# Performance work log

Hardware: AMD Instinct MI355X
Metric: run time of the kernel (lower is better)

Reference implementation:

```python
import jax, jax.numpy as jnp
import numpy as np

MAX_LEN = 512   # static padding cap for the ragged sequences
EPS = 1e-12     # F.normalize default eps


def setup_inputs() -> dict:
    key = jax.random.key(0)
    ks = jax.random.split(key, 6)
    B, T, D, H = 2048, 262144, 64, 128
    x = jax.random.normal(ks[0], (T, D), jnp.float32)
    offsets = jnp.sort(jax.random.randint(ks[1], (B,), 0, T)).astype(jnp.int64)
    offsets = offsets.at[0].set(0)  # first segment starts at 0 as in EmbeddingLookup
    W_ih = jax.random.normal(ks[2], (3 * H, D), jnp.float32) * 0.1   # [r,z,n] stacked
    W_hh = jax.random.normal(ks[3], (3 * H, H), jnp.float32) * 0.1
    W_dense = jax.random.normal(ks[4], (D, H), jnp.float32) * 0.1
    b_dense = jax.random.normal(ks[5], (D,), jnp.float32) * 0.1
    return {"x": x, "offsets": offsets, "W_ih": W_ih, "W_hh": W_hh,
            "W_dense": W_dense, "b_dense": b_dense}


def _forward(x, W_ih, W_hh, W_dense, b_dense, offsets):
    T, D = x.shape
    B = offsets.shape[0]
    H = W_hh.shape[1]
    # segment lengths as in get_field_embedding_list: diffs + trailing segment
    lengths = jnp.concatenate([offsets[1:] - offsets[:-1], T - offsets[-1:]])
    lengths = jnp.clip(lengths, 1, MAX_LEN)
    # ragged -> padded [B, L, D] (pad_sequence equivalent)
    t_idx = jnp.arange(MAX_LEN)
    gidx = jnp.clip(offsets[:, None] + t_idx[None, :], 0, T - 1)      # [B, L]
    mask = (t_idx[None, :] < lengths[:, None]).astype(x.dtype)        # [B, L]
    padded = x[gidx] * mask[:, :, None]                               # [B, L, D]
    # single-layer GRU, bias=False, batch_first; scan over time
    xs = jnp.transpose(padded, (1, 0, 2))                             # [L, B, D]

    def step(h, x_t):
        gi = x_t @ W_ih.T                                             # [B, 3H]
        gh = h @ W_hh.T                                               # [B, 3H]
        ir, iz, inn = jnp.split(gi, 3, axis=-1)
        hr, hz, hn = jnp.split(gh, 3, axis=-1)
        r = jax.nn.sigmoid(ir + hr)
        z = jax.nn.sigmoid(iz + hz)
        n = jnp.tanh(inn + r * hn)
        h_new = (1.0 - z) * n + z * h
        return h_new, h_new

    h0 = jnp.zeros((B, H), x.dtype)
    _, ys = jax.lax.scan(step, h0, xs)                                # [L, B, H]
    gru_out = jnp.transpose(ys, (1, 0, 2))                            # [B, L, H]
    # gather_indexes: hidden state at last valid timestep
    last = gru_out[jnp.arange(B), lengths - 1]                        # [B, H]
    out = last @ W_dense.T + b_dense                                  # [B, D]
    norm = jnp.linalg.norm(out, axis=-1, keepdims=True)
    return out / jnp.maximum(norm, EPS)


def reference(x, offsets, W_ih, W_hh, W_dense, b_dense):
    return _forward(x, W_ih, W_hh, W_dense, b_dense, offsets)
```

## Files before the change

kernel.cpp:

```cpp
#include <hip/hip_runtime.h>
#include <math.h>

constexpr int D = 64;
constexpr int H = 128;
constexpr int MAXLEN = 512;
constexpr int MSEQ = 8;

typedef __attribute__((ext_vector_type(8))) short short8;
typedef __attribute__((ext_vector_type(4))) float f32x4;

__device__ __forceinline__ short f2bf(float f) {
    unsigned u = __float_as_uint(f);
    u += 0x7fffu + ((u >> 16) & 1u);
    return (short)(u >> 16);
}
__device__ __forceinline__ unsigned cvtpk(float a, float b) {
    unsigned r;
    asm volatile("v_cvt_pk_bf16_f32 %0, %1, %2" : "=v"(r) : "v"(a), "v"(b));
    return r;
}
__device__ __forceinline__ short8 pack8(float4 a, float4 b) {
    short8 r;
    r[0]=f2bf(a.x); r[1]=f2bf(a.y); r[2]=f2bf(a.z); r[3]=f2bf(a.w);
    r[4]=f2bf(b.x); r[5]=f2bf(b.y); r[6]=f2bf(b.z); r[7]=f2bf(b.w);
    return r;
}
__device__ __forceinline__ float rcp_(float x) { return __builtin_amdgcn_rcpf(x); }
__device__ __forceinline__ float sig_(float v) { return rcp_(1.0f + __expf(-v)); }
__device__ __forceinline__ float tanh_(float v) {
    float a = fabsf(v);
    float e = __expf(2.0f * a);
    float t = 1.0f - 2.0f * rcp_(e + 1.0f);
    return copysignf(t, v);
}
__device__ __forceinline__ void lgkm_barrier() {
    asm volatile("s_waitcnt lgkmcnt(0)\n\ts_barrier" ::: "memory");
}

#define MFMA(a,b,c) __builtin_amdgcn_mfma_f32_16x16x32_bf16((a),(b),(c),0,0,0)

__global__ __launch_bounds__(256, 1)
void gru_w4(const float* __restrict__ x,
            const int* __restrict__ offsets,
            const float* __restrict__ W_ih,
            const float* __restrict__ W_hh,
            const float* __restrict__ W_dense,
            const float* __restrict__ b_dense,
            float* __restrict__ out,
            int B, int T)
{
    const int bb   = blockIdx.x;
    const int tid  = threadIdx.x;
    const int w    = tid >> 6;
    const int l    = tid & 63;
    const int s    = l & 15;
    const int q    = l >> 4;
    const int sq   = s & 7;
    const int hsel = s >> 3;

    __shared__ __align__(16) short h_bf[2][MSEQ * H];
    __shared__ __align__(16) short x_bf[2][MSEQ * D];
    __shared__ int slen[MSEQ], sstart[MSEQ];
    __shared__ float h_f32[MSEQ][H];

    if (tid < MSEQ) {
        int sg = bb * MSEQ + tid;
        int st = 0, en = 1;
        if (sg < B) { st = offsets[sg]; en = (sg + 1 < B) ? offsets[sg + 1] : T; }
        int ln = en - st;
        ln = max(1, min(ln, MAXLEN));
        sstart[tid] = st; slen[tid] = ln;
    }
    {
        int* hz = (int*)h_bf[0];
        hz[tid] = 0; hz[tid + 256] = 0;
    }
    __syncthreads();

    int nt = 1;
#pragma unroll
    for (int i = 0; i < MSEQ; ++i) nt = max(nt, slen[i]);

    short8 Wh[3][2][4];
    short8 Wi[3][2][2];
#pragma unroll
    for (int g = 0; g < 3; ++g) {
#pragma unroll
        for (int u = 0; u < 2; ++u) {
            const int grow = g * H + w * 32 + u * 16 + s;
            const float* ph = W_hh + (size_t)grow * H + q * 8;
#pragma unroll
            for (int kt = 0; kt < 4; ++kt)
                Wh[g][u][kt] = pack8(*(const float4*)(ph + kt * 32),
                                     *(const float4*)(ph + kt * 32 + 4));
            const float* pi = W_ih + (size_t)grow * D + q * 8;
#pragma unroll
            for (int kt = 0; kt < 2; ++kt)
                Wi[g][u][kt] = pack8(*(const float4*)(pi + kt * 32),
                                     *(const float4*)(pi + kt * 32 + 4));
        }
    }

    int hoff[4], xoff[2], woff[2];
#pragma unroll
    for (int kt = 0; kt < 4; ++kt) hoff[kt] = sq * 256 + (((kt * 4 + q) ^ sq) << 4);
#pragma unroll
    for (int kt = 0; kt < 2; ++kt) xoff[kt] = sq * 128 + (((kt * 4 + q) ^ sq) << 4);
#pragma unroll
    for (int u = 0; u < 2; ++u)
        woff[u] = sq * 256 + ((((4 * w) + (2 * u) + (q >> 1)) ^ sq) << 4)
                + ((q & 1) << 3) + (hsel << 2);

    const int ss  = tid >> 5;
    const int pxx = tid & 31;
    const int st_x = sstart[ss];
    const int ln_x = slen[ss];
    const float* xg = x + (size_t)st_x * D + pxx * 2;
    const int xwoff = ss * 128 + (((pxx >> 2) ^ ss) << 4) + ((pxx & 3) << 2);

    {
        float2 v = *(const float2*)xg;
        *(unsigned*)((char*)x_bf[0] + xwoff) = cvtpk(v.x, v.y);
    }
    float2 xpf = *(const float2*)(xg + (size_t)min(1, ln_x - 1) * D);

    const int ln_s = slen[sq];
    float h00 = 0.f, h01 = 0.f;
    float h10 = 0.f, h11 = 0.f;

    __syncthreads();

    for (int t = 0; t < nt; ++t) {
        const int p = t & 1;
        const char* hb = (const char*)h_bf[p];
        const char* xb = (const char*)x_bf[p];

        short8 bh[4], bx[2];
#pragma unroll
        for (int kt = 0; kt < 4; ++kt) bh[kt] = *(const short8*)(hb + hoff[kt]);
#pragma unroll
        for (int kt = 0; kt < 2; ++kt) bx[kt] = *(const short8*)(xb + xoff[kt]);

        float2 xnew;
        {
            const int tn = (t + 2 < ln_x) ? t + 2 : ln_x - 1;
            xnew = *(const float2*)(xg + (size_t)tn * D);
        }

        f32x4 cr[2] = {{0,0,0,0},{0,0,0,0}};
        f32x4 cz[2] = {{0,0,0,0},{0,0,0,0}};
        f32x4 ci[2] = {{0,0,0,0},{0,0,0,0}};
        f32x4 chh[2]= {{0,0,0,0},{0,0,0,0}};
#pragma unroll
        for (int u = 0; u < 2; ++u) {
#pragma unroll
            for (int kt = 0; kt < 2; ++kt) {
                cr[u] = MFMA(Wi[0][u][kt], bx[kt], cr[u]);
                cz[u] = MFMA(Wi[1][u][kt], bx[kt], cz[u]);
                ci[u] = MFMA(Wi[2][u][kt], bx[kt], ci[u]);
            }
#pragma unroll
            for (int kt = 0; kt < 4; ++kt) {
                cr[u]  = MFMA(Wh[0][u][kt], bh[kt], cr[u]);
                cz[u]  = MFMA(Wh[1][u][kt], bh[kt], cz[u]);
                chh[u] = MFMA(Wh[2][u][kt], bh[kt], chh[u]);
            }
        }

        const bool upd = (t < ln_s);
        {
            float vr0 = hsel ? cr[0][2]  : cr[0][0],  vr1 = hsel ? cr[0][3]  : cr[0][1];
            float vz0 = hsel ? cz[0][2]  : cz[0][0],  vz1 = hsel ? cz[0][3]  : cz[0][1];
            float vi0 = hsel ? ci[0][2]  : ci[0][0],  vi1 = hsel ? ci[0][3]  : ci[0][1];
            float vh0 = hsel ? chh[0][2] : chh[0][0], vh1 = hsel ? chh[0][3] : chh[0][1];
            float r0 = sig_(vr0), r1 = sig_(vr1);
            float z0 = sig_(vz0), z1 = sig_(vz1);
            float n0 = tanh_(vi0 + r0 * vh0);
            float n1 = tanh_(vi1 + r1 * vh1);
            float a0 = (1.0f - z0) * n0 + z0 * h00;
            float a1 = (1.0f - z1) * n1 + z1 * h01;
            h00 = upd ? a0 : h00;
            h01 = upd ? a1 : h01;
        }
        {
            float vr0 = hsel ? cr[1][2]  : cr[1][0],  vr1 = hsel ? cr[1][3]  : cr[1][1];
            float vz0 = hsel ? cz[1][2]  : cz[1][0],  vz1 = hsel ? cz[1][3]  : cz[1][1];
            float vi0 = hsel ? ci[1][2]  : ci[1][0],  vi1 = hsel ? ci[1][3]  : ci[1][1];
            float vh0 = hsel ? chh[1][2] : chh[1][0], vh1 = hsel ? chh[1][3] : chh[1][1];
            float r0 = sig_(vr0), r1 = sig_(vr1);
            float z0 = sig_(vz0), z1 = sig_(vz1);
            float n0 = tanh_(vi0 + r0 * vh0);
            float n1 = tanh_(vi1 + r1 * vh1);
            float a0 = (1.0f - z0) * n0 + z0 * h10;
            float a1 = (1.0f - z1) * n1 + z1 * h11;
            h10 = upd ? a0 : h10;
            h11 = upd ? a1 : h11;
        }

        *(unsigned*)((char*)h_bf[p ^ 1] + woff[0]) = cvtpk(h00, h01);
        *(unsigned*)((char*)h_bf[p ^ 1] + woff[1]) = cvtpk(h10, h11);
        *(unsigned*)((char*)x_bf[p ^ 1] + xwoff)   = cvtpk(xpf.x, xpf.y);
        xpf = xnew;

        lgkm_barrier();
    }

    {
        float2 hv0 = { h00, h01 };
        float2 hv1 = { h10, h11 };
        *(float2*)&h_f32[sq][w * 32 + 0  + q * 4 + 2 * hsel] = hv0;
        *(float2*)&h_f32[sq][w * 32 + 16 + q * 4 + 2 * hsel] = hv1;
    }
    __syncthreads();

    {
        const int s2 = tid >> 5;
        const int cb = tid & 31;
        float acc0 = b_dense[cb];
        float acc1 = b_dense[cb + 32];
        const float* w0 = W_dense + (size_t)cb * H;
        const float* w1 = W_dense + (size_t)(cb + 32) * H;
#pragma unroll
        for (int j = 0; j < H; j += 4) {
            float4 hv = *(const float4*)&h_f32[s2][j];
            float4 a0 = *(const float4*)(w0 + j);
            float4 a1 = *(const float4*)(w1 + j);
            acc0 += hv.x*a0.x + hv.y*a0.y + hv.z*a0.z + hv.w*a0.w;
            acc1 += hv.x*a1.x + hv.y*a1.y + hv.z*a1.z + hv.w*a1.w;
        }
        float s2q = acc0 * acc0 + acc1 * acc1;
#pragma unroll
        for (int off = 16; off >= 1; off >>= 1) s2q += __shfl_xor(s2q, off);
        float invn = 1.0f / fmaxf(sqrtf(s2q), 1e-12f);
        int sg = bb * MSEQ + s2;
        if (sg < B) {
            out[(size_t)sg * D + cb]      = acc0 * invn;
            out[(size_t)sg * D + cb + 32] = acc1 * invn;
        }
    }
}

extern "C" void kernel_launch(void* const* d_in, const int* in_sizes, int n_in,
                              void* d_out, int out_size, void* d_ws, size_t ws_size,
                              hipStream_t stream) {
    const float* x       = (const float*)d_in[0];
    const int*   offsets = (const int*)d_in[1];
    const float* W_ih    = (const float*)d_in[2];
    const float* W_hh    = (const float*)d_in[3];
    const float* W_dense = (const float*)d_in[4];
    const float* b_dense = (const float*)d_in[5];
    float*       out     = (float*)d_out;

    const int B = in_sizes[1];
    const int T = in_sizes[0] / D;
    const int grid = (B + MSEQ - 1) / MSEQ;

    gru_w4<<<grid, 256, 0, stream>>>(x, offsets, W_ih, W_hh, W_dense, b_dense, out, B, T);
}
```

Before: 352.6 us.

## Precompute next-step input projections off the GRU recurrence critical path

Moves the x·W_ih MFMAs for step t+1 to after the gate update of step t, so that each step's dependent path holds only the h·W_hh MFMAs. The x staging buffer is now filled one step further ahead, with two slots primed before the loop and the global prefetch pushed to t+3. The gate accumulators are seeded with the precomputed input projections. The cost is more live accumulator registers and a deeper prefetch with its own edge-case indexing.

```diff
diff --git a/kernel.cpp b/kernel.cpp
--- a/kernel.cpp
+++ b/kernel.cpp
@@ -40,7 +40,7 @@
 #define MFMA(a,b,c) __builtin_amdgcn_mfma_f32_16x16x32_bf16((a),(b),(c),0,0,0)
 
 __global__ __launch_bounds__(256, 1)
-void gru_w4(const float* __restrict__ x,
+void gru_p4(const float* __restrict__ x,
             const int* __restrict__ offsets,
             const float* __restrict__ W_ih,
             const float* __restrict__ W_hh,
@@ -119,10 +119,12 @@
     const int xwoff = ss * 128 + (((pxx >> 2) ^ ss) << 4) + ((pxx & 3) << 2);
 
     {
-        float2 v = *(const float2*)xg;
-        *(unsigned*)((char*)x_bf[0] + xwoff) = cvtpk(v.x, v.y);
-    }
-    float2 xpf = *(const float2*)(xg + (size_t)min(1, ln_x - 1) * D);
+        float2 v0 = *(const float2*)xg;
+        float2 v1 = *(const float2*)(xg + (size_t)min(1, ln_x - 1) * D);
+        *(unsigned*)((char*)x_bf[0] + xwoff) = cvtpk(v0.x, v0.y);
+        *(unsigned*)((char*)x_bf[1] + xwoff) = cvtpk(v1.x, v1.y);
+    }
+    float2 xpf = *(const float2*)(xg + (size_t)min(2, ln_x - 1) * D);
 
     const int ln_s = slen[sq];
     float h00 = 0.f, h01 = 0.f;
@@ -130,49 +132,55 @@
 
     __syncthreads();
 
+    const f32x4 zf = {0.f, 0.f, 0.f, 0.f};
+    f32x4 gr[2], gz[2], gn[2];
+    {
+        short8 bx0[2];
+#pragma unroll
+        for (int kt = 0; kt < 2; ++kt)
+            bx0[kt] = *(const short8*)((const char*)x_bf[0] + xoff[kt]);
+#pragma unroll
+        for (int u = 0; u < 2; ++u) {
+            gr[u] = MFMA(Wi[0][u][0], bx0[0], zf);
+            gr[u] = MFMA(Wi[0][u][1], bx0[1], gr[u]);
+            gz[u] = MFMA(Wi[1][u][0], bx0[0], zf);
+            gz[u] = MFMA(Wi[1][u][1], bx0[1], gz[u]);
+            gn[u] = MFMA(Wi[2][u][0], bx0[0], zf);
+            gn[u] = MFMA(Wi[2][u][1], bx0[1], gn[u]);
+        }
+    }
+    lgkm_barrier();
+
     for (int t = 0; t < nt; ++t) {
         const int p = t & 1;
         const char* hb = (const char*)h_bf[p];
-        const char* xb = (const char*)x_bf[p];
-
-        short8 bh[4], bx[2];
+        const char* xb = (const char*)x_bf[p ^ 1];
+
+        short8 bh[4], bxn[2];
 #pragma unroll
         for (int kt = 0; kt < 4; ++kt) bh[kt] = *(const short8*)(hb + hoff[kt]);
 #pragma unroll
-        for (int kt = 0; kt < 2; ++kt) bx[kt] = *(const short8*)(xb + xoff[kt]);
-
-        float2 xnew;
-        {
-            const int tn = (t + 2 < ln_x) ? t + 2 : ln_x - 1;
-            xnew = *(const float2*)(xg + (size_t)tn * D);
-        }
-
-        f32x4 cr[2] = {{0,0,0,0},{0,0,0,0}};
-        f32x4 cz[2] = {{0,0,0,0},{0,0,0,0}};
-        f32x4 ci[2] = {{0,0,0,0},{0,0,0,0}};
-        f32x4 chh[2]= {{0,0,0,0},{0,0,0,0}};
-#pragma unroll
-        for (int u = 0; u < 2; ++u) {
-#pragma unroll
-            for (int kt = 0; kt < 2; ++kt) {
-                cr[u] = MFMA(Wi[0][u][kt], bx[kt], cr[u]);
-                cz[u] = MFMA(Wi[1][u][kt], bx[kt], cz[u]);
-                ci[u] = MFMA(Wi[2][u][kt], bx[kt], ci[u]);
-            }
+        for (int kt = 0; kt < 2; ++kt) bxn[kt] = *(const short8*)(xb + xoff[kt]);
+
+        f32x4 chn[2];
+#pragma unroll
+        for (int u = 0; u < 2; ++u) {
+            chn[u] = MFMA(Wh[2][u][0], bh[0], zf);
+#pragma unroll
+            for (int kt = 1; kt < 4; ++kt) chn[u] = MFMA(Wh[2][u][kt], bh[kt], chn[u]);
 #pragma unroll
             for (int kt = 0; kt < 4; ++kt) {
-                cr[u]  = MFMA(Wh[0][u][kt], bh[kt], cr[u]);
-                cz[u]  = MFMA(Wh[1][u][kt], bh[kt], cz[u]);
-                chh[u] = MFMA(Wh[2][u][kt], bh[kt], chh[u]);
+                gr[u] = MFMA(Wh[0][u][kt], bh[kt], gr[u]);
+                gz[u] = MFMA(Wh[1][u][kt], bh[kt], gz[u]);
             }
         }
 
         const bool upd = (t < ln_s);
         {
-            float vr0 = hsel ? cr[0][2]  : cr[0][0],  vr1 = hsel ? cr[0][3]  : cr[0][1];
-            float vz0 = hsel ? cz[0][2]  : cz[0][0],  vz1 = hsel ? cz[0][3]  : cz[0][1];
-            float vi0 = hsel ? ci[0][2]  : ci[0][0],  vi1 = hsel ? ci[0][3]  : ci[0][1];
-            float vh0 = hsel ? chh[0][2] : chh[0][0], vh1 = hsel ? chh[0][3] : chh[0][1];
+            float vr0 = hsel ? gr[0][2] : gr[0][0], vr1 = hsel ? gr[0][3] : gr[0][1];
+            float vz0 = hsel ? gz[0][2] : gz[0][0], vz1 = hsel ? gz[0][3] : gz[0][1];
+            float vi0 = hsel ? gn[0][2] : gn[0][0], vi1 = hsel ? gn[0][3] : gn[0][1];
+            float vh0 = hsel ? chn[0][2] : chn[0][0], vh1 = hsel ? chn[0][3] : chn[0][1];
             float r0 = sig_(vr0), r1 = sig_(vr1);
             float z0 = sig_(vz0), z1 = sig_(vz1);
             float n0 = tanh_(vi0 + r0 * vh0);
@@ -183,10 +191,10 @@
             h01 = upd ? a1 : h01;
         }
         {
-            float vr0 = hsel ? cr[1][2]  : cr[1][0],  vr1 = hsel ? cr[1][3]  : cr[1][1];
-            float vz0 = hsel ? cz[1][2]  : cz[1][0],  vz1 = hsel ? cz[1][3]  : cz[1][1];
-            float vi0 = hsel ? ci[1][2]  : ci[1][0],  vi1 = hsel ? ci[1][3]  : ci[1][1];
-            float vh0 = hsel ? chh[1][2] : chh[1][0], vh1 = hsel ? chh[1][3] : chh[1][1];
+            float vr0 = hsel ? gr[1][2] : gr[1][0], vr1 = hsel ? gr[1][3] : gr[1][1];
+            float vz0 = hsel ? gz[1][2] : gz[1][0], vz1 = hsel ? gz[1][3] : gz[1][1];
+            float vi0 = hsel ? gn[1][2] : gn[1][0], vi1 = hsel ? gn[1][3] : gn[1][1];
+            float vh0 = hsel ? chn[1][2] : chn[1][0], vh1 = hsel ? chn[1][3] : chn[1][1];
             float r0 = sig_(vr0), r1 = sig_(vr1);
             float z0 = sig_(vz0), z1 = sig_(vz1);
             float n0 = tanh_(vi0 + r0 * vh0);
@@ -199,8 +207,22 @@
 
         *(unsigned*)((char*)h_bf[p ^ 1] + woff[0]) = cvtpk(h00, h01);
         *(unsigned*)((char*)h_bf[p ^ 1] + woff[1]) = cvtpk(h10, h11);
-        *(unsigned*)((char*)x_bf[p ^ 1] + xwoff)   = cvtpk(xpf.x, xpf.y);
-        xpf = xnew;
+
+#pragma unroll
+        for (int u = 0; u < 2; ++u) {
+            gr[u] = MFMA(Wi[0][u][0], bxn[0], zf);
+            gr[u] = MFMA(Wi[0][u][1], bxn[1], gr[u]);
+            gz[u] = MFMA(Wi[1][u][0], bxn[0], zf);
+            gz[u] = MFMA(Wi[1][u][1], bxn[1], gz[u]);
+            gn[u] = MFMA(Wi[2][u][0], bxn[0], zf);
+            gn[u] = MFMA(Wi[2][u][1], bxn[1], gn[u]);
+        }
+
+        *(unsigned*)((char*)x_bf[p] + xwoff) = cvtpk(xpf.x, xpf.y);
+        {
+            const int tn = (t + 3 < ln_x) ? t + 3 : ln_x - 1;
+            xpf = *(const float2*)(xg + (size_t)tn * D);
+        }
 
         lgkm_barrier();
     }
@@ -255,5 +277,5 @@
     const int T = in_sizes[0] / D;
     const int grid = (B + MSEQ - 1) / MSEQ;
 
-    gru_w4<<<grid, 256, 0, stream>>>(x, offsets, W_ih, W_hh, W_dense, b_dense, out, B, T);
-}
+    gru_p4<<<grid, 256, 0, stream>>>(x, offsets, W_ih, W_hh, W_dense, b_dense, out, B, T);
+}
```

Measured after the change: 341.6 us. 1.03x faster.
